# Optimization experiments

Hardware: AMD Instinct MI355X
Metric: run time of the kernel (lower is better)

The kernel has to match this reference:

```python
import jax, jax.numpy as jnp
import numpy as np

LN_EPS = 1e-5

def setup_inputs() -> dict:
    key = jax.random.key(0)
    ks = jax.random.split(key, 12)
    B, S, M, C, D = 16, 1024, 4096, 768, 256
    inp = {
        'seed_xyz_norm': jax.random.normal(ks[0], (B, S, 3), jnp.float32),
        'p_last': jax.random.normal(ks[1], (B, M, 3), jnp.float32),
        'f_last': jax.random.normal(ks[2], (B, C, M), jnp.float32),
        'seed_features': jax.random.normal(ks[3], (B, D, S), jnp.float32),
        # LayerNorm params over C
        'ln_gamma': jnp.ones((C,), jnp.float32),
        'ln_beta': jnp.zeros((C,), jnp.float32),
        # conv1d projector C -> 256 (kernel size 1) + ReLU
        'proj_w': jax.random.normal(ks[4], (D, C), jnp.float32) * (1.0 / np.sqrt(C)),
        'proj_b': jnp.zeros((D,), jnp.float32),
        # fusion MLP: concat512 -> 512 -> 256 (1x1 convs)
        'mlp_w1': jax.random.normal(ks[5], (2 * D, 2 * D), jnp.float32) * (1.0 / np.sqrt(2 * D)),
        'mlp_b1': jnp.zeros((2 * D,), jnp.float32),
        'mlp_w2': jax.random.normal(ks[6], (D, 2 * D), jnp.float32) * (1.0 / np.sqrt(2 * D)),
        'mlp_b2': jnp.zeros((D,), jnp.float32),
    }
    return inp


def reference(seed_xyz_norm, p_last, f_last, seed_features,
              ln_gamma, ln_beta, proj_w, proj_b,
              mlp_w1, mlp_b1, mlp_w2, mlp_b2):
    # --- nearest_neighbor_gather_features ---
    # squared distance [B,S,M]; argmin over M, gather features [B,C,S]
    d2 = jnp.sum(seed_xyz_norm * seed_xyz_norm, -1, keepdims=True) \
         - 2.0 * jnp.einsum('bsd,bmd->bsm', seed_xyz_norm, p_last) \
         + jnp.sum(p_last * p_last, -1)[:, None, :]
    idx = jnp.argmin(d2, axis=-1)                                   # [B,S]
    lift3d_raw = jnp.take_along_axis(f_last, idx[:, None, :], axis=2)  # [B,C,S]

    # --- LayerNorm over channel dim C ---
    mu = jnp.mean(lift3d_raw, axis=1, keepdims=True)
    var = jnp.mean((lift3d_raw - mu) ** 2, axis=1, keepdims=True)
    x_ln = (lift3d_raw - mu) * jax.lax.rsqrt(var + LN_EPS)
    x_ln = x_ln * ln_gamma[None, :, None] + ln_beta[None, :, None]

    # --- conv1d projector (1x1) + ReLU ---
    proj = jax.nn.relu(jnp.einsum('oc,bcs->bos', proj_w, x_ln) + proj_b[None, :, None])

    # --- concat fusion MLP ---
    fused = jnp.concatenate([seed_features, proj], axis=1)          # [B,512,S]
    h = jax.nn.relu(jnp.einsum('oc,bcs->bos', mlp_w1, fused) + mlp_b1[None, :, None])
    mixed = jnp.einsum('oc,bcs->bos', mlp_w2, h) + mlp_b2[None, :, None]  # [B,256,S]
    return mixed
```

## Files before the change

kernel.cpp:

```cpp
#include <hip/hip_runtime.h>

namespace {

constexpr int B = 16, S = 1024, M = 4096, C = 768, D = 256;

typedef __attribute__((ext_vector_type(8))) short bf16x8;
typedef __attribute__((ext_vector_type(4))) float f32x4;

__device__ inline ushort f2bf(float f) {
  uint u = __float_as_uint(f);
  uint r = (u + 0x7FFFu + ((u >> 16) & 1u)) >> 16;
  return (ushort)r;
}

__global__ __launch_bounds__(256)
void nn_kernel(const float* __restrict__ xyz, const float* __restrict__ p,
               int* __restrict__ idx_out) {
  const int b = blockIdx.y;
  const int t = threadIdx.x;
  const int seed = blockIdx.x * 16 + (t >> 4);
  const int l16 = t & 15;

  const float sx = xyz[((size_t)b * S + seed) * 3 + 0];
  const float sy = xyz[((size_t)b * S + seed) * 3 + 1];
  const float sz = xyz[((size_t)b * S + seed) * 3 + 2];
  const float ss = __fadd_rn(__fadd_rn(__fmul_rn(sx, sx), __fmul_rn(sy, sy)),
                             __fmul_rn(sz, sz));

  __shared__ float px[256], py[256], pz[256], pp[256];

  float best = 3.4028235e38f;
  int besti = 0;
  const float* pb = p + (size_t)b * M * 3;

  for (int m0 = 0; m0 < M; m0 += 256) {
    __syncthreads();
    {
      const float a0 = pb[(size_t)(m0 + t) * 3 + 0];
      const float a1 = pb[(size_t)(m0 + t) * 3 + 1];
      const float a2 = pb[(size_t)(m0 + t) * 3 + 2];
      px[t] = a0; py[t] = a1; pz[t] = a2;
      pp[t] = __fadd_rn(__fadd_rn(__fmul_rn(a0, a0), __fmul_rn(a1, a1)),
                        __fmul_rn(a2, a2));
    }
    __syncthreads();
    #pragma unroll 4
    for (int j = l16; j < 256; j += 16) {
      float dot = __fmul_rn(sx, px[j]);
      dot = __fadd_rn(dot, __fmul_rn(sy, py[j]));
      dot = __fadd_rn(dot, __fmul_rn(sz, pz[j]));
      const float d2 = __fadd_rn(__fsub_rn(ss, __fmul_rn(2.0f, dot)), pp[j]);
      const int mi = m0 + j;
      if (d2 < best || (d2 == best && mi < besti)) { best = d2; besti = mi; }
    }
  }
  #pragma unroll
  for (int off = 8; off >= 1; off >>= 1) {
    const float ob = __shfl_xor(best, off, 16);
    const int   oi = __shfl_xor(besti, off, 16);
    if (ob < best || (ob == best && oi < besti)) { best = ob; besti = oi; }
  }
  if (l16 == 0) idx_out[b * S + seed] = besti;
}

__global__ __launch_bounds__(512)
void sort_kernel(const int* __restrict__ idx, int* __restrict__ sIdx,
                 int* __restrict__ sS) {
  const int b = blockIdx.x;
  const int t = threadIdx.x;
  __shared__ int key[1024];
  __shared__ int val[1024];
  key[t] = idx[b * S + t];         val[t] = t;
  key[t + 512] = idx[b * S + t + 512]; val[t + 512] = t + 512;
  __syncthreads();
  for (int k = 2; k <= 1024; k <<= 1) {
    for (int j = k >> 1; j > 0; j >>= 1) {
      #pragma unroll 2
      for (int i = t; i < 1024; i += 512) {
        const int p = i ^ j;
        if (p > i) {
          const bool up = ((i & k) == 0);
          const int ki = key[i], kp = key[p];
          if ((ki > kp) == up) {
            key[i] = kp; key[p] = ki;
            const int tv = val[i]; val[i] = val[p]; val[p] = tv;
          }
        }
      }
      __syncthreads();
    }
  }
  sIdx[b * S + t] = key[t];       sS[b * S + t] = val[t];
  sIdx[b * S + t + 512] = key[t + 512]; sS[b * S + t + 512] = val[t + 512];
}

__global__ __launch_bounds__(256)
void gather_ln_kernel(const float* __restrict__ f, const int* __restrict__ sIdx,
                      const int* __restrict__ sS,
                      const float* __restrict__ gamma, const float* __restrict__ beta,
                      ushort* __restrict__ xln) {
  const int b = blockIdx.y;
  const int rl = blockIdx.x;
  const int r = ((rl & 7) << 7) + (rl >> 3);
  const int t = threadIdx.x;
  const int s = sS[b * S + r];
  const int m = sIdx[b * S + r];

  const float* fb = f + (size_t)b * C * M + m;
  const float v0 = fb[(size_t)(t      ) * M];
  const float v1 = fb[(size_t)(t + 256) * M];
  const float v2 = fb[(size_t)(t + 512) * M];

  __shared__ float red[4];
  __shared__ float stats[2];
  const int wave = t >> 6;

  float ps = v0 + v1 + v2;
  #pragma unroll
  for (int off = 32; off >= 1; off >>= 1) ps += __shfl_xor(ps, off);
  if ((t & 63) == 0) red[wave] = ps;
  __syncthreads();
  if (t == 0) stats[0] = (red[0] + red[1] + red[2] + red[3]) * (1.0f / 768.0f);
  __syncthreads();
  const float mu = stats[0];

  const float d0 = v0 - mu, d1 = v1 - mu, d2 = v2 - mu;
  float pv = d0 * d0 + d1 * d1 + d2 * d2;
  #pragma unroll
  for (int off = 32; off >= 1; off >>= 1) pv += __shfl_xor(pv, off);
  if ((t & 63) == 0) red[wave] = pv;
  __syncthreads();
  if (t == 0) {
    const float var = (red[0] + red[1] + red[2] + red[3]) * (1.0f / 768.0f);
    stats[1] = 1.0f / sqrtf(var + 1e-5f);
  }
  __syncthreads();
  const float rs = stats[1];

  ushort* ob = xln + ((size_t)b * S + s) * C;
  ob[t      ] = f2bf((d0 * rs) * gamma[t      ] + beta[t      ]);
  ob[t + 256] = f2bf((d1 * rs) * gamma[t + 256] + beta[t + 256]);
  ob[t + 512] = f2bf((d2 * rs) * gamma[t + 512] + beta[t + 512]);
}

__global__ __launch_bounds__(256)
void transpose_sf_kernel(const float* __restrict__ sf, ushort* __restrict__ fused) {
  const int b = blockIdx.z;
  const int d0 = blockIdx.y * 64;
  const int s0 = blockIdx.x * 64;
  const int t = threadIdx.x;
  __shared__ float tile[64][68];

  const float* inb = sf + ((size_t)b * D + d0) * S + s0;
  #pragma unroll
  for (int q = 0; q < 4; ++q) {
    const int rr = (t >> 4) + q * 16;
    const int c4 = (t & 15) * 4;
    const float4 v = *(const float4*)&inb[(size_t)rr * S + c4];
    *(float4*)&tile[rr][c4] = v;
  }
  __syncthreads();
  #pragma unroll
  for (int q = 0; q < 4; ++q) {
    const int srow = (t >> 4) + q * 16;
    const int dc = (t & 15) * 4;
    ushort4 o;
    o.x = f2bf(tile[dc + 0][srow]);
    o.y = f2bf(tile[dc + 1][srow]);
    o.z = f2bf(tile[dc + 2][srow]);
    o.w = f2bf(tile[dc + 3][srow]);
    *(ushort4*)&fused[((size_t)b * S + s0 + srow) * 512 + d0 + dc] = o;
  }
}

__global__ __launch_bounds__(256)
void convert_w_kernel(const float* __restrict__ w0, int n0, ushort* __restrict__ o0,
                      const float* __restrict__ w1, int n1, ushort* __restrict__ o1,
                      const float* __restrict__ w2, int n2, ushort* __restrict__ o2) {
  const int which = blockIdx.y;
  const float* src = which == 0 ? w0 : which == 1 ? w1 : w2;
  ushort* dst = which == 0 ? o0 : which == 1 ? o1 : o2;
  const int n = which == 0 ? n0 : which == 1 ? n1 : n2;
  const int i = (blockIdx.x * 256 + threadIdx.x) * 4;
  if (i < n) {
    const float4 v = *(const float4*)&src[i];
    ushort4 o;
    o.x = f2bf(v.x); o.y = f2bf(v.y); o.z = f2bf(v.z); o.w = f2bf(v.w);
    *(ushort4*)&dst[i] = o;
  }
}

__global__ __launch_bounds__(256)
void gemm_bf16_kernel(const ushort* __restrict__ W, int K, int O,
                      const ushort* __restrict__ X,
                      const float* __restrict__ bias,
                      void* __restrict__ out, int outMode, int ldOut, int colOff,
                      int relu) {
  const int b  = blockIdx.z;
  const int s0 = blockIdx.x * 128;
  const int o0 = blockIdx.y * 128;
  const int t  = threadIdx.x;
  const int wave = t >> 6;
  const int lane = t & 63;
  const int l16 = lane & 15;
  const int quad = lane >> 4;

  __shared__ ushort Wt[128 * 40];
  __shared__ ushort Xt[128 * 40];
  __shared__ float biasS[128];

  if (t < 128) biasS[t] = bias[o0 + t];

  f32x4 acc[8][2];
  const f32x4 z = {0.f, 0.f, 0.f, 0.f};
  #pragma unroll
  for (int of = 0; of < 8; ++of) { acc[of][0] = z; acc[of][1] = z; }

  const ushort* Xb = X + (size_t)b * S * K;
  const int kg = t & 3;
  const int row = t >> 2;

  for (int c0 = 0; c0 < K; c0 += 32) {
    __syncthreads();
    #pragma unroll
    for (int q = 0; q < 2; ++q) {
      const int rr = row + 64 * q;
      const uint4 wv = *(const uint4*)&W[(size_t)(o0 + rr) * K + c0 + kg * 8];
      *(uint4*)&Wt[rr * 40 + kg * 8] = wv;
      const uint4 xv = *(const uint4*)&Xb[(size_t)(s0 + rr) * K + c0 + kg * 8];
      *(uint4*)&Xt[rr * 40 + kg * 8] = xv;
    }
    __syncthreads();

    bf16x8 bfr[2];
    #pragma unroll
    for (int sf = 0; sf < 2; ++sf)
      bfr[sf] = *(const bf16x8*)&Xt[(wave * 32 + sf * 16 + l16) * 40 + quad * 8];
    #pragma unroll
    for (int of = 0; of < 8; ++of) {
      const bf16x8 afr = *(const bf16x8*)&Wt[(of * 16 + l16) * 40 + quad * 8];
      acc[of][0] = __builtin_amdgcn_mfma_f32_16x16x32_bf16(afr, bfr[0], acc[of][0], 0, 0, 0);
      acc[of][1] = __builtin_amdgcn_mfma_f32_16x16x32_bf16(afr, bfr[1], acc[of][1], 0, 0, 0);
    }
  }

  if (outMode == 0) {
    ushort* ob = (ushort*)out;
    #pragma unroll
    for (int of = 0; of < 8; ++of) {
      #pragma unroll
      for (int sf = 0; sf < 2; ++sf) {
        const int s = s0 + wave * 32 + sf * 16 + l16;
        const int ol = of * 16 + quad * 4;
        float v0 = acc[of][sf].x + biasS[ol + 0];
        float v1 = acc[of][sf].y + biasS[ol + 1];
        float v2 = acc[of][sf].z + biasS[ol + 2];
        float v3 = acc[of][sf].w + biasS[ol + 3];
        if (relu) {
          v0 = fmaxf(v0, 0.f); v1 = fmaxf(v1, 0.f);
          v2 = fmaxf(v2, 0.f); v3 = fmaxf(v3, 0.f);
        }
        ushort4 st;
        st.x = f2bf(v0); st.y = f2bf(v1); st.z = f2bf(v2); st.w = f2bf(v3);
        *(ushort4*)&ob[((size_t)b * S + s) * ldOut + colOff + o0 + ol] = st;
      }
    }
  } else {
    float* o32 = (float*)out;
    #pragma unroll
    for (int of = 0; of < 8; ++of) {
      #pragma unroll
      for (int sf = 0; sf < 2; ++sf) {
        const int s = s0 + wave * 32 + sf * 16 + l16;
        const int ol = of * 16 + quad * 4;
        const float vr[4] = {acc[of][sf].x, acc[of][sf].y, acc[of][sf].z, acc[of][sf].w};
        #pragma unroll
        for (int r = 0; r < 4; ++r) {
          const int o = o0 + ol + r;
          o32[((size_t)b * O + o) * S + s] = vr[r] + biasS[ol + r];
        }
      }
    }
  }
}

}

extern "C" void kernel_launch(void* const* d_in, const int* in_sizes, int n_in,
                              void* d_out, int out_size, void* d_ws, size_t ws_size,
                              hipStream_t stream) {
  const float* seed_xyz  = (const float*)d_in[0];
  const float* p_last    = (const float*)d_in[1];
  const float* f_last    = (const float*)d_in[2];
  const float* seed_feat = (const float*)d_in[3];
  const float* ln_gamma  = (const float*)d_in[4];
  const float* ln_beta   = (const float*)d_in[5];
  const float* proj_w    = (const float*)d_in[6];
  const float* proj_b    = (const float*)d_in[7];
  const float* mlp_w1    = (const float*)d_in[8];
  const float* mlp_b1    = (const float*)d_in[9];
  const float* mlp_w2    = (const float*)d_in[10];
  const float* mlp_b2    = (const float*)d_in[11];
  float* out = (float*)d_out;

  char* ws = (char*)d_ws;
  int*    idx   = (int*)(ws);
  int*    sIdx  = (int*)(ws + (64 << 10));
  int*    sS    = (int*)(ws + (128 << 10));
  ushort* wp_bf = (ushort*)(ws + (256 << 10));
  ushort* w1_bf = (ushort*)(ws + (640 << 10));
  ushort* w2_bf = (ushort*)(ws + (1152 << 10));
  ushort* xln   = (ushort*)(ws + (2ull << 20));
  ushort* fused = (ushort*)(ws + (26ull << 20));
  ushort* hbuf  = (ushort*)(ws + (42ull << 20));

  nn_kernel<<<dim3(S / 16, B), 256, 0, stream>>>(seed_xyz, p_last, idx);
  sort_kernel<<<dim3(B), 512, 0, stream>>>(idx, sIdx, sS);

  gather_ln_kernel<<<dim3(S, B), 256, 0, stream>>>(f_last, sIdx, sS,
                                                   ln_gamma, ln_beta, xln);

  transpose_sf_kernel<<<dim3(S / 64, D / 64, B), 256, 0, stream>>>(seed_feat, fused);
  convert_w_kernel<<<dim3(256, 3), 256, 0, stream>>>(
      proj_w, D * C, wp_bf, mlp_w1, 512 * 512, w1_bf, mlp_w2, 256 * 512, w2_bf);

  gemm_bf16_kernel<<<dim3(S / 128, 256 / 128, B), 256, 0, stream>>>(
      wp_bf, C, 256, xln, proj_b, fused, 0, 512, 256, 1);

  gemm_bf16_kernel<<<dim3(S / 128, 512 / 128, B), 256, 0, stream>>>(
      w1_bf, 512, 512, fused, mlp_b1, hbuf, 0, 512, 0, 1);

  gemm_bf16_kernel<<<dim3(S / 128, 256 / 128, B), 256, 0, stream>>>(
      w2_bf, 512, 256, hbuf, mlp_b2, out, 1, 0, 0, 0);
}
```

Measured before the change: 436.3 us.

## Pack point data, bucket-sort indices, gather two rows per block, prefetch GEMM tiles

Nearest-neighbour point data is packed into one float4 per point in shared memory, so each candidate takes one LDS load instead of four. The bitonic sort of indices becomes a shared-memory counting sort into 256 buckets of 16 points each, which keeps gather locality without full ordering. The gather+LayerNorm kernel now handles two seeds per block to get more memory-level parallelism and fewer barriers per row. The GEMM adds register prefetch of the next K tile so global loads overlap with the MFMA work.

Result: faster. 410.0 us (-6.0%).

```diff
diff --git a/kernel.cpp b/kernel.cpp
--- a/kernel.cpp
+++ b/kernel.cpp
@@ -27,7 +27,7 @@
   const float ss = __fadd_rn(__fadd_rn(__fmul_rn(sx, sx), __fmul_rn(sy, sy)),
                              __fmul_rn(sz, sz));
 
-  __shared__ float px[256], py[256], pz[256], pp[256];
+  __shared__ float4 pt[256];
 
   float best = 3.4028235e38f;
   int besti = 0;
@@ -39,17 +39,18 @@
       const float a0 = pb[(size_t)(m0 + t) * 3 + 0];
       const float a1 = pb[(size_t)(m0 + t) * 3 + 1];
       const float a2 = pb[(size_t)(m0 + t) * 3 + 2];
-      px[t] = a0; py[t] = a1; pz[t] = a2;
-      pp[t] = __fadd_rn(__fadd_rn(__fmul_rn(a0, a0), __fmul_rn(a1, a1)),
-                        __fmul_rn(a2, a2));
+      const float pp = __fadd_rn(__fadd_rn(__fmul_rn(a0, a0), __fmul_rn(a1, a1)),
+                                 __fmul_rn(a2, a2));
+      pt[t] = make_float4(a0, a1, a2, pp);
     }
     __syncthreads();
     #pragma unroll 4
     for (int j = l16; j < 256; j += 16) {
-      float dot = __fmul_rn(sx, px[j]);
-      dot = __fadd_rn(dot, __fmul_rn(sy, py[j]));
-      dot = __fadd_rn(dot, __fmul_rn(sz, pz[j]));
-      const float d2 = __fadd_rn(__fsub_rn(ss, __fmul_rn(2.0f, dot)), pp[j]);
+      const float4 q = pt[j];
+      float dot = __fmul_rn(sx, q.x);
+      dot = __fadd_rn(dot, __fmul_rn(sy, q.y));
+      dot = __fadd_rn(dot, __fmul_rn(sz, q.z));
+      const float d2 = __fadd_rn(__fsub_rn(ss, __fmul_rn(2.0f, dot)), q.w);
       const int mi = m0 + j;
       if (d2 < best || (d2 == best && mi < besti)) { best = d2; besti = mi; }
     }
@@ -63,35 +64,50 @@
   if (l16 == 0) idx_out[b * S + seed] = besti;
 }
 
-__global__ __launch_bounds__(512)
-void sort_kernel(const int* __restrict__ idx, int* __restrict__ sIdx,
-                 int* __restrict__ sS) {
+__global__ __launch_bounds__(256)
+void bucket_sort_kernel(const int* __restrict__ idx, int* __restrict__ sIdx,
+                        int* __restrict__ sS) {
   const int b = blockIdx.x;
   const int t = threadIdx.x;
-  __shared__ int key[1024];
-  __shared__ int val[1024];
-  key[t] = idx[b * S + t];         val[t] = t;
-  key[t + 512] = idx[b * S + t + 512]; val[t + 512] = t + 512;
-  __syncthreads();
-  for (int k = 2; k <= 1024; k <<= 1) {
-    for (int j = k >> 1; j > 0; j >>= 1) {
-      #pragma unroll 2
-      for (int i = t; i < 1024; i += 512) {
-        const int p = i ^ j;
-        if (p > i) {
-          const bool up = ((i & k) == 0);
-          const int ki = key[i], kp = key[p];
-          if ((ki > kp) == up) {
-            key[i] = kp; key[p] = ki;
-            const int tv = val[i]; val[i] = val[p]; val[p] = tv;
-          }
-        }
-      }
-      __syncthreads();
-    }
-  }
-  sIdx[b * S + t] = key[t];       sS[b * S + t] = val[t];
-  sIdx[b * S + t + 512] = key[t + 512]; sS[b * S + t + 512] = val[t + 512];
+  __shared__ int keys[1024];
+  __shared__ int cnt[256];
+  __shared__ int base[256];
+  __shared__ int wsum[4];
+
+  cnt[t] = 0;
+  #pragma unroll
+  for (int i = 0; i < 4; ++i) keys[t + 256 * i] = idx[b * S + t + 256 * i];
+  __syncthreads();
+  #pragma unroll
+  for (int i = 0; i < 4; ++i) atomicAdd(&cnt[keys[t + 256 * i] >> 4], 1);
+  __syncthreads();
+
+  const int v = cnt[t];
+  int sc = v;
+  #pragma unroll
+  for (int off = 1; off < 64; off <<= 1) {
+    const int o = __shfl_up(sc, off);
+    if ((t & 63) >= off) sc += o;
+  }
+  if ((t & 63) == 63) wsum[t >> 6] = sc;
+  __syncthreads();
+  int wb = 0;
+  #pragma unroll
+  for (int w = 0; w < 4; ++w)
+    if (w < (t >> 6)) wb += wsum[w];
+  base[t] = wb + sc - v;
+  cnt[t] = 0;
+  __syncthreads();
+
+  #pragma unroll
+  for (int i = 0; i < 4; ++i) {
+    const int s = t + 256 * i;
+    const int m = keys[s];
+    const int bu = m >> 4;
+    const int r = base[bu] + atomicAdd(&cnt[bu], 1);
+    sIdx[b * S + r] = m;
+    sS[b * S + r] = s;
+  }
 }
 
 __global__ __launch_bounds__(256)
@@ -101,46 +117,69 @@
                       ushort* __restrict__ xln) {
   const int b = blockIdx.y;
   const int rl = blockIdx.x;
-  const int r = ((rl & 7) << 7) + (rl >> 3);
+  const int r0 = (((rl & 7) << 6) + (rl >> 3)) << 1;
   const int t = threadIdx.x;
-  const int s = sS[b * S + r];
-  const int m = sIdx[b * S + r];
-
-  const float* fb = f + (size_t)b * C * M + m;
-  const float v0 = fb[(size_t)(t      ) * M];
-  const float v1 = fb[(size_t)(t + 256) * M];
-  const float v2 = fb[(size_t)(t + 512) * M];
-
-  __shared__ float red[4];
-  __shared__ float stats[2];
+  const int sA = sS[b * S + r0],     mA = sIdx[b * S + r0];
+  const int sB = sS[b * S + r0 + 1], mB = sIdx[b * S + r0 + 1];
+
+  const float* fb = f + (size_t)b * C * M;
+  const float a0 = fb[(size_t)(t      ) * M + mA];
+  const float a1 = fb[(size_t)(t + 256) * M + mA];
+  const float a2 = fb[(size_t)(t + 512) * M + mA];
+  const float c0 = fb[(size_t)(t      ) * M + mB];
+  const float c1 = fb[(size_t)(t + 256) * M + mB];
+  const float c2 = fb[(size_t)(t + 512) * M + mB];
+
+  const float g0 = gamma[t], g1 = gamma[t + 256], g2 = gamma[t + 512];
+  const float e0 = beta[t],  e1 = beta[t + 256],  e2 = beta[t + 512];
+
+  __shared__ float redA[4], redB[4], stats[4];
   const int wave = t >> 6;
 
-  float ps = v0 + v1 + v2;
-  #pragma unroll
-  for (int off = 32; off >= 1; off >>= 1) ps += __shfl_xor(ps, off);
-  if ((t & 63) == 0) red[wave] = ps;
-  __syncthreads();
-  if (t == 0) stats[0] = (red[0] + red[1] + red[2] + red[3]) * (1.0f / 768.0f);
-  __syncthreads();
-  const float mu = stats[0];
-
-  const float d0 = v0 - mu, d1 = v1 - mu, d2 = v2 - mu;
-  float pv = d0 * d0 + d1 * d1 + d2 * d2;
-  #pragma unroll
-  for (int off = 32; off >= 1; off >>= 1) pv += __shfl_xor(pv, off);
-  if ((t & 63) == 0) red[wave] = pv;
+  float psA = a0 + a1 + a2;
+  float psB = c0 + c1 + c2;
+  #pragma unroll
+  for (int off = 32; off >= 1; off >>= 1) {
+    psA += __shfl_xor(psA, off);
+    psB += __shfl_xor(psB, off);
+  }
+  if ((t & 63) == 0) { redA[wave] = psA; redB[wave] = psB; }
   __syncthreads();
   if (t == 0) {
-    const float var = (red[0] + red[1] + red[2] + red[3]) * (1.0f / 768.0f);
-    stats[1] = 1.0f / sqrtf(var + 1e-5f);
-  }
-  __syncthreads();
-  const float rs = stats[1];
-
-  ushort* ob = xln + ((size_t)b * S + s) * C;
-  ob[t      ] = f2bf((d0 * rs) * gamma[t      ] + beta[t      ]);
-  ob[t + 256] = f2bf((d1 * rs) * gamma[t + 256] + beta[t + 256]);
-  ob[t + 512] = f2bf((d2 * rs) * gamma[t + 512] + beta[t + 512]);
+    stats[0] = (redA[0] + redA[1] + redA[2] + redA[3]) * (1.0f / 768.0f);
+    stats[1] = (redB[0] + redB[1] + redB[2] + redB[3]) * (1.0f / 768.0f);
+  }
+  __syncthreads();
+  const float muA = stats[0], muB = stats[1];
+
+  const float dA0 = a0 - muA, dA1 = a1 - muA, dA2 = a2 - muA;
+  const float dB0 = c0 - muB, dB1 = c1 - muB, dB2 = c2 - muB;
+  float pvA = dA0 * dA0 + dA1 * dA1 + dA2 * dA2;
+  float pvB = dB0 * dB0 + dB1 * dB1 + dB2 * dB2;
+  #pragma unroll
+  for (int off = 32; off >= 1; off >>= 1) {
+    pvA += __shfl_xor(pvA, off);
+    pvB += __shfl_xor(pvB, off);
+  }
+  if ((t & 63) == 0) { redA[wave] = pvA; redB[wave] = pvB; }
+  __syncthreads();
+  if (t == 0) {
+    const float varA = (redA[0] + redA[1] + redA[2] + redA[3]) * (1.0f / 768.0f);
+    const float varB = (redB[0] + redB[1] + redB[2] + redB[3]) * (1.0f / 768.0f);
+    stats[2] = 1.0f / sqrtf(varA + 1e-5f);
+    stats[3] = 1.0f / sqrtf(varB + 1e-5f);
+  }
+  __syncthreads();
+  const float rsA = stats[2], rsB = stats[3];
+
+  ushort* oA = xln + ((size_t)b * S + sA) * C;
+  ushort* oB = xln + ((size_t)b * S + sB) * C;
+  oA[t      ] = f2bf((dA0 * rsA) * g0 + e0);
+  oA[t + 256] = f2bf((dA1 * rsA) * g1 + e1);
+  oA[t + 512] = f2bf((dA2 * rsA) * g2 + e2);
+  oB[t      ] = f2bf((dB0 * rsB) * g0 + e0);
+  oB[t + 256] = f2bf((dB1 * rsB) * g1 + e1);
+  oB[t + 512] = f2bf((dB2 * rsB) * g2 + e2);
 }
 
 __global__ __launch_bounds__(256)
@@ -219,18 +258,30 @@
   const ushort* Xb = X + (size_t)b * S * K;
   const int kg = t & 3;
   const int row = t >> 2;
+  const size_t wBase = (size_t)(o0 + row) * K + kg * 8;
+  const size_t xBase = (size_t)(s0 + row) * K + kg * 8;
+  const size_t wBase2 = wBase + (size_t)64 * K;
+  const size_t xBase2 = xBase + (size_t)64 * K;
+
+  uint4 wv0 = *(const uint4*)&W[wBase];
+  uint4 wv1 = *(const uint4*)&W[wBase2];
+  uint4 xv0 = *(const uint4*)&Xb[xBase];
+  uint4 xv1 = *(const uint4*)&Xb[xBase2];
 
   for (int c0 = 0; c0 < K; c0 += 32) {
     __syncthreads();
-    #pragma unroll
-    for (int q = 0; q < 2; ++q) {
-      const int rr = row + 64 * q;
-      const uint4 wv = *(const uint4*)&W[(size_t)(o0 + rr) * K + c0 + kg * 8];
-      *(uint4*)&Wt[rr * 40 + kg * 8] = wv;
-      const uint4 xv = *(const uint4*)&Xb[(size_t)(s0 + rr) * K + c0 + kg * 8];
-      *(uint4*)&Xt[rr * 40 + kg * 8] = xv;
-    }
+    *(uint4*)&Wt[row * 40 + kg * 8] = wv0;
+    *(uint4*)&Wt[(row + 64) * 40 + kg * 8] = wv1;
+    *(uint4*)&Xt[row * 40 + kg * 8] = xv0;
+    *(uint4*)&Xt[(row + 64) * 40 + kg * 8] = xv1;
     __syncthreads();
+
+    if (c0 + 32 < K) {
+      wv0 = *(const uint4*)&W[wBase + c0 + 32];
+      wv1 = *(const uint4*)&W[wBase2 + c0 + 32];
+      xv0 = *(const uint4*)&Xb[xBase + c0 + 32];
+      xv1 = *(const uint4*)&Xb[xBase2 + c0 + 32];
+    }
 
     bf16x8 bfr[2];
     #pragma unroll
@@ -315,10 +366,10 @@
   ushort* hbuf  = (ushort*)(ws + (42ull << 20));
 
   nn_kernel<<<dim3(S / 16, B), 256, 0, stream>>>(seed_xyz, p_last, idx);
-  sort_kernel<<<dim3(B), 512, 0, stream>>>(idx, sIdx, sS);
-
-  gather_ln_kernel<<<dim3(S, B), 256, 0, stream>>>(f_last, sIdx, sS,
-                                                   ln_gamma, ln_beta, xln);
+  bucket_sort_kernel<<<dim3(B), 256, 0, stream>>>(idx, sIdx, sS);
+
+  gather_ln_kernel<<<dim3(S / 2, B), 256, 0, stream>>>(f_last, sIdx, sS,
+                                                       ln_gamma, ln_beta, xln);
 
   transpose_sf_kernel<<<dim3(S / 64, D / 64, B), 256, 0, stream>>>(seed_feat, fused);
   convert_w_kernel<<<dim3(256, 3), 256, 0, stream>>>(
```
